# Optimization experiments

Hardware: AMD Instinct MI355X
Metric: run time of the kernel (lower is better)

The kernel has to match this reference:

```python
import jax, jax.numpy as jnp
import numpy as np

B, L, D, H = 2, 2048, 1024, 16
DK = D // H


def setup_inputs() -> dict:
    key = jax.random.key(0)
    ks = jax.random.split(key, 12)
    s = 1.0 / np.sqrt(D)
    return {
        "x": jax.random.normal(ks[0], (B, L, D), jnp.float32),
        "timestamps": jnp.sort(jax.random.uniform(ks[1], (B, L), jnp.float32) * 1000.0, axis=-1),
        "decay_values": jax.random.normal(ks[2], (B, L), jnp.float32),
        "pad_mask": jnp.ones((B, L), dtype=bool),
        "Wq": jax.random.normal(ks[3], (D, D), jnp.float32) * s,
        "bq": jnp.zeros((D,), jnp.float32),
        "Wk": jax.random.normal(ks[4], (D, D), jnp.float32) * s,
        "bk": jnp.zeros((D,), jnp.float32),
        "Wv": jax.random.normal(ks[5], (D, D), jnp.float32) * s,
        "bv": jnp.zeros((D,), jnp.float32),
        "Wo": jax.random.normal(ks[6], (D, D), jnp.float32) * s,
        "bo": jnp.zeros((D,), jnp.float32),
        "lam": jnp.float32(0.01),
    }


def reference(x, timestamps, decay_values, pad_mask, Wq, bq, Wk, bk, Wv, bv, Wo, bo, lam):
    b, l, d = x.shape
    # projections (torch Linear: x @ W.T + b), split heads -> [B,H,L,DK]
    def split_heads(y):
        return y.reshape(b, l, H, DK).transpose(0, 2, 1, 3)
    Q = split_heads(x @ Wq.T + bq)
    K = split_heads(x @ Wk.T + bk)
    V = split_heads(x @ Wv.T + bv)

    scores = jnp.einsum("bhqd,bhkd->bhqk", Q, K) / np.sqrt(DK)
    # temporal log-decay bias
    t_diff = jnp.abs(timestamps[:, :, None] - timestamps[:, None, :])  # [B,L,L]
    denom = jax.lax.stop_gradient(jnp.maximum(t_diff.max(), 1.0))  # matches .item() constant
    scores = scores - jnp.abs(lam) * jnp.log1p(t_diff / denom)[:, None, :, :]

    causal = jnp.triu(jnp.ones((l, l), dtype=bool), k=1)  # True above diag -> masked
    neg_inf = jnp.float32(-jnp.inf)
    scores = jnp.where(causal[None, None], neg_inf, scores)
    scores = jnp.where(pad_mask[:, None, None, :], scores, neg_inf)

    attn = jnp.nan_to_num(jax.nn.softmax(scores, axis=-1), nan=0.0)
    out = jnp.einsum("bhqk,bhkd->bhqd", attn, V)
    out = out.transpose(0, 2, 1, 3).reshape(b, l, d)
    return out @ Wo.T + bo
```

## Files before the change

kernel.cpp:

```cpp
#include <hip/hip_runtime.h>
#include <hip/hip_bf16.h>
#include <math.h>

#define Bsz 2
#define Lsz 2048
#define Dsz 1024
#define Hsz 16
#define DKsz 64
#define NW_ELEMS (1u << 20)

typedef __attribute__((ext_vector_type(8))) short short8;
typedef __attribute__((ext_vector_type(4))) float v4f;
typedef unsigned short ushortT;
#define MFMA16(a, b, c) __builtin_amdgcn_mfma_f32_16x16x32_bf16(a, b, c, 0, 0, 0)
#define LOG2E 1.44269504088896340736f

__device__ __forceinline__ ushortT f2bf(float f) {
    union { float f; unsigned u; } x; x.f = f;
    unsigned r = x.u + 0x7fffu + ((x.u >> 16) & 1u);
    return (ushortT)(r >> 16);
}
__device__ __forceinline__ float bf2f(ushortT s) {
    union { unsigned u; float f; } x; x.u = ((unsigned)s) << 16;
    return x.f;
}
__device__ __forceinline__ void glds16(const void* g, void* l) {
    __builtin_amdgcn_global_load_lds(
        (const __attribute__((address_space(1))) void*)g,
        (__attribute__((address_space(3))) void*)l, 16, 0, 0);
}

__global__ __launch_bounds__(256) void cast_all(const float* __restrict__ x,
                                                const float* __restrict__ Wq,
                                                const float* __restrict__ Wk,
                                                const float* __restrict__ Wv,
                                                const float* __restrict__ Wo,
                                                ushortT* __restrict__ xb,
                                                ushortT* __restrict__ Wqkvb,
                                                ushortT* __restrict__ Wob) {
    const int NX = Bsz * Lsz * Dsz;
    int i = (blockIdx.x * 256 + threadIdx.x) * 4;
    const float* src; ushortT* dst;
    if (i < NX) { src = x + i; dst = xb + i; }
    else {
        int j = i - NX;
        if (j < 3 * (int)NW_ELEMS) {
            int w = j >> 20, o = j & (NW_ELEMS - 1);
            src = (w == 0 ? Wq : (w == 1 ? Wk : Wv)) + o;
            dst = Wqkvb + j;
        } else {
            int o = j - 3 * NW_ELEMS;
            src = Wo + o; dst = Wob + o;
        }
    }
    float4 v = *(const float4*)src;
    ushort4 o4;
    o4.x = f2bf(v.x); o4.y = f2bf(v.y); o4.z = f2bf(v.z); o4.w = f2bf(v.w);
    *(ushort4*)dst = o4;
}

__global__ __launch_bounds__(256) void denom_bias_kernel(const float* __restrict__ t,
                                                         const float* __restrict__ bq,
                                                         const float* __restrict__ bk,
                                                         const float* __restrict__ bv,
                                                         float* __restrict__ out,
                                                         float* __restrict__ cbias) {
    __shared__ float smx[256], smn[256];
    int tid = threadIdx.x;
    for (int i = tid; i < 3 * Dsz; i += 256)
        cbias[i] = (i < Dsz) ? bq[i] : (i < 2 * Dsz ? bk[i - Dsz] : bv[i - 2 * Dsz]);
    float best = 1.0f;
    for (int b = 0; b < Bsz; ++b) {
        float mx = -INFINITY, mn = INFINITY;
        for (int i = tid; i < Lsz; i += 256) {
            float v = t[b * Lsz + i];
            mx = fmaxf(mx, v);
            mn = fminf(mn, v);
        }
        smx[tid] = mx; smn[tid] = mn;
        __syncthreads();
        for (int s = 128; s > 0; s >>= 1) {
            if (tid < s) {
                smx[tid] = fmaxf(smx[tid], smx[tid + s]);
                smn[tid] = fminf(smn[tid], smn[tid + s]);
            }
            __syncthreads();
        }
        best = fmaxf(best, smx[0] - smn[0]);
        __syncthreads();
    }
    if (tid == 0) out[0] = best;
}

template <bool QKV>
__global__ __launch_bounds__(256) void gemm_mfma(const ushortT* __restrict__ A,
                                                 const ushortT* __restrict__ W,
                                                 const float* __restrict__ bias,
                                                 void* __restrict__ O0,
                                                 void* __restrict__ O1,
                                                 void* __restrict__ O2) {
    const int K = Dsz;
    __shared__ ushortT As[128 * 32];
    __shared__ ushortT Ws[128 * 32];
    int tid = threadIdx.x;
    int wid = tid >> 6, lane = tid & 63, quad = lane >> 4, m16 = lane & 15;
    int wm = wid >> 1, wn = wid & 1;
    int m0 = blockIdx.y * 128, n0 = blockIdx.x * 128;
    int lrow = lane >> 2, lcol = (lane & 3) * 8;

    v4f acc[4][4];
#pragma unroll
    for (int i = 0; i < 4; ++i)
#pragma unroll
        for (int j = 0; j < 4; ++j) acc[i][j] = (v4f){0.f, 0.f, 0.f, 0.f};

    for (int kt = 0; kt < K; kt += 32) {
        __syncthreads();
#pragma unroll
        for (int hf = 0; hf < 2; ++hf) {
            int r0 = wid * 32 + hf * 16;
            const ushortT* ga = A + (size_t)(m0 + r0 + lrow) * K + kt + lcol;
            const ushortT* gw = W + (size_t)(n0 + r0 + lrow) * K + kt + lcol;
            glds16(ga, &As[r0 * 32]);
            glds16(gw, &Ws[r0 * 32]);
        }
        __syncthreads();
        short8 af[4], wf[4];
#pragma unroll
        for (int mt = 0; mt < 4; ++mt)
            af[mt] = *(const short8*)&As[(wm * 64 + mt * 16 + m16) * 32 + quad * 8];
#pragma unroll
        for (int nt = 0; nt < 4; ++nt)
            wf[nt] = *(const short8*)&Ws[(wn * 64 + nt * 16 + m16) * 32 + quad * 8];
#pragma unroll
        for (int mt = 0; mt < 4; ++mt)
#pragma unroll
            for (int nt = 0; nt < 4; ++nt)
                acc[mt][nt] = MFMA16(af[mt], wf[nt], acc[mt][nt]);
    }

    if (QKV) {
        int region = n0 >> 10;
        float scale = (region == 0) ? 0.125f * LOG2E : 1.0f;
#pragma unroll
        for (int nt = 0; nt < 4; ++nt) {
            int col = n0 + wn * 64 + nt * 16 + m16;
            float bv_ = bias[col];
            int c1 = col & (Dsz - 1);
#pragma unroll
            for (int mt = 0; mt < 4; ++mt) {
                int row0 = m0 + wm * 64 + mt * 16 + quad * 4;
                if (region == 2) {
                    ushort4 pk;
                    pk.x = f2bf(acc[mt][nt][0] + bv_);
                    pk.y = f2bf(acc[mt][nt][1] + bv_);
                    pk.z = f2bf(acc[mt][nt][2] + bv_);
                    pk.w = f2bf(acc[mt][nt][3] + bv_);
                    int bb = row0 >> 11, seq = row0 & (Lsz - 1);
                    *(ushort4*)&((ushortT*)O2)[((size_t)bb * Dsz + c1) * Lsz + seq] = pk;
                } else {
                    ushortT* dst = (ushortT*)(region == 0 ? O0 : O1);
#pragma unroll
                    for (int r = 0; r < 4; ++r)
                        dst[(size_t)(row0 + r) * Dsz + c1] =
                            f2bf((acc[mt][nt][r] + bv_) * scale);
                }
            }
        }
    } else {
#pragma unroll
        for (int nt = 0; nt < 4; ++nt) {
            int col = n0 + wn * 64 + nt * 16 + m16;
            float bv_ = bias[col];
#pragma unroll
            for (int mt = 0; mt < 4; ++mt) {
                int row0 = m0 + wm * 64 + mt * 16 + quad * 4;
#pragma unroll
                for (int r = 0; r < 4; ++r)
                    ((float*)O0)[(size_t)(row0 + r) * Dsz + col] = acc[mt][nt][r] + bv_;
            }
        }
    }
}

__global__ __launch_bounds__(512) void attn_mfma(const ushortT* __restrict__ Qb,
                                                 const ushortT* __restrict__ Kb,
                                                 const ushortT* __restrict__ Vtg,
                                                 const float* __restrict__ ts,
                                                 const float* __restrict__ denomp,
                                                 const float* __restrict__ lamp,
                                                 ushortT* __restrict__ AOb) {
    int pid = blockIdx.x;
    int h = blockIdx.y, b = blockIdx.z;
    int tid = threadIdx.x;
    int wid = tid >> 6, lane = tid & 63, quad = lane >> 4, m16 = lane & 15;

    __shared__ ushortT Ks[64 * 72];
    __shared__ ushortT Vs[64 * 72];
    __shared__ ushortT Pl[8][16 * 72];
    __shared__ float tks[64];

    float denom = denomp[0];
    float alam = fabsf(lamp[0]);
    float c0 = alam * __builtin_amdgcn_logf(denom);
    const size_t bL = (size_t)b * Lsz;

    int sr = tid >> 3, sc = (tid & 7) * 8;

    for (int half = 0; half < 2; ++half) {
        int qt = half ? (15 - pid) : pid;
        int q0 = qt * 128;
        int ntiles = 2 * (qt + 1);
        int jd = 2 * qt + (wid >> 2);

        int qrow = q0 + wid * 16 + m16;
        const ushortT* qptr = Qb + (bL + qrow) * Dsz + h * 64 + quad * 8;
        short8 qf0 = *(const short8*)qptr;
        short8 qf1 = *(const short8*)(qptr + 32);

        float tq[4];
        int gq[4];
#pragma unroll
        for (int r = 0; r < 4; ++r) {
            gq[r] = q0 + wid * 16 + quad * 4 + r;
            tq[r] = ts[bL + gq[r]];
        }

        v4f o[4];
        float lacc[4];
#pragma unroll
        for (int i = 0; i < 4; ++i) { o[i] = (v4f){0.f, 0.f, 0.f, 0.f}; lacc[i] = 0.f; }

        uint4 kv, vv;
        float tkv = 0.f;
        {
            const ushortT* ksrc = Kb + (bL + sr) * Dsz + h * 64 + sc;
            const ushortT* vsrc = Vtg + ((size_t)b * Dsz + h * 64 + sr) * Lsz + sc;
            kv = *(const uint4*)ksrc;
            vv = *(const uint4*)vsrc;
            if (tid < 64) tkv = ts[bL + tid];
        }

        for (int jt = 0; jt < ntiles; ++jt) {
            int k0 = jt * 64;
            __syncthreads();
            *(uint4*)&Ks[sr * 72 + sc] = kv;
            *(uint4*)&Vs[sr * 72 + sc] = vv;
            if (tid < 64) tks[tid] = tkv;
            __syncthreads();
            if (jt + 1 < ntiles) {
                int k1 = k0 + 64;
                const ushortT* ksrc = Kb + (bL + k1 + sr) * Dsz + h * 64 + sc;
                const ushortT* vsrc = Vtg + ((size_t)b * Dsz + h * 64 + sr) * Lsz + k1 + sc;
                kv = *(const uint4*)ksrc;
                vv = *(const uint4*)vsrc;
                if (tid < 64) tkv = ts[bL + k1 + tid];
            }
            if (jt > jd) continue;

            v4f s[4];
#pragma unroll
            for (int ct = 0; ct < 4; ++ct) {
                short8 kf0 = *(const short8*)&Ks[(ct * 16 + m16) * 72 + quad * 8];
                short8 kf1 = *(const short8*)&Ks[(ct * 16 + m16) * 72 + 32 + quad * 8];
                s[ct] = (v4f){0.f, 0.f, 0.f, 0.f};
                s[ct] = MFMA16(qf0, kf0, s[ct]);
                s[ct] = MFMA16(qf1, kf1, s[ct]);
            }

            bool diag = (jt == jd);
#pragma unroll
            for (int ct = 0; ct < 4; ++ct) {
                int gk = k0 + ct * 16 + m16;
                float tk = tks[ct * 16 + m16];
#pragma unroll
                for (int r = 0; r < 4; ++r) {
                    float w = denom + fabsf(tq[r] - tk);
                    float f = s[ct][r] + fmaf(-alam, __builtin_amdgcn_logf(w), c0);
                    if (diag) f = (gk <= gq[r]) ? f : -INFINITY;
                    float p = __builtin_amdgcn_exp2f(f);
                    ushortT pb = f2bf(p);
                    Pl[wid][(quad * 4 + r) * 72 + ct * 16 + m16] = pb;
                    lacc[r] += bf2f(pb);
                }
            }

            short8 pf0 = *(const short8*)&Pl[wid][m16 * 72 + quad * 8];
            short8 pf1 = *(const short8*)&Pl[wid][m16 * 72 + 32 + quad * 8];
#pragma unroll
            for (int dt = 0; dt < 4; ++dt) {
                short8 vf0 = *(const short8*)&Vs[(dt * 16 + m16) * 72 + quad * 8];
                short8 vf1 = *(const short8*)&Vs[(dt * 16 + m16) * 72 + 32 + quad * 8];
                o[dt] = MFMA16(pf0, vf0, o[dt]);
                o[dt] = MFMA16(pf1, vf1, o[dt]);
            }
        }

#pragma unroll
        for (int r = 0; r < 4; ++r) {
            float l = lacc[r];
#pragma unroll
            for (int off = 1; off < 16; off <<= 1)
                l += __shfl_xor(l, off, 16);
            float invl = 1.0f / l;
#pragma unroll
            for (int dt = 0; dt < 4; ++dt) {
                int col = h * 64 + dt * 16 + m16;
                AOb[(bL + gq[r]) * Dsz + col] = f2bf(o[dt][r] * invl);
            }
        }
    }
}

extern "C" void kernel_launch(void* const* d_in, const int* in_sizes, int n_in,
                              void* d_out, int out_size, void* d_ws, size_t ws_size,
                              hipStream_t stream) {
    const float* x   = (const float*)d_in[0];
    const float* ts  = (const float*)d_in[1];
    const float* Wq  = (const float*)d_in[4];
    const float* bq  = (const float*)d_in[5];
    const float* Wk  = (const float*)d_in[6];
    const float* bk  = (const float*)d_in[7];
    const float* Wv  = (const float*)d_in[8];
    const float* bv  = (const float*)d_in[9];
    const float* Wo  = (const float*)d_in[10];
    const float* bo  = (const float*)d_in[11];
    const float* lam = (const float*)d_in[12];

    const size_t NX = (size_t)Bsz * Lsz * Dsz;
    const size_t NW = (size_t)NW_ELEMS;

    char* w = (char*)d_ws;
    float* denom = (float*)w;            w += 256;
    float* cbias = (float*)w;            w += 3 * Dsz * 4 + 256;
    ushortT* xb    = (ushortT*)w;        w += NX * 2;
    ushortT* Wqkvb = (ushortT*)w;        w += 3 * NW * 2;
    ushortT* Wob   = (ushortT*)w;        w += NW * 2;
    ushortT* Qb    = (ushortT*)w;        w += NX * 2;
    ushortT* Kbf   = (ushortT*)w;        w += NX * 2;
    ushortT* Vtg   = (ushortT*)w;        w += NX * 2;
    ushortT* AOb   = (ushortT*)w;        w += NX * 2;

    denom_bias_kernel<<<1, 256, 0, stream>>>(ts, bq, bk, bv, denom, cbias);

    int cast_blocks = (int)((NX + 4 * NW) / 4 / 256);
    cast_all<<<cast_blocks, 256, 0, stream>>>(x, Wq, Wk, Wv, Wo, xb, Wqkvb, Wob);

    dim3 gqkv(3 * Dsz / 128, (Bsz * Lsz) / 128);
    gemm_mfma<true><<<gqkv, 256, 0, stream>>>(xb, Wqkvb, cbias, Qb, Kbf, Vtg);

    dim3 ablk(8, Hsz, Bsz);
    attn_mfma<<<ablk, 512, 0, stream>>>(Qb, Kbf, Vtg, ts, denom, lam, AOb);

    dim3 gout(Dsz / 128, (Bsz * Lsz) / 128);
    gemm_mfma<false><<<gout, 256, 0, stream>>>(AOb, Wob, bo, d_out, nullptr, nullptr);
}
```

Baseline: 242.9 us.

## Shrink attention blocks to 64-row tiles and fuse denom into cast kernel

The attention kernel moves from 512-thread blocks over 128-query tiles to 256-thread blocks over 64-query tiles, doubling the grid and removing idle warps that skipped the last key tile. The denominator/bias reduction runs as an extra block of the cast kernel, saving one launch. The bf16 conversion of probabilities now truncates instead of rounding to nearest, and the bias add is folded into a single FMA. Truncation changes numerics slightly, and the smaller blocks reload K/V tiles more often per query.

```diff
diff --git a/kernel.cpp b/kernel.cpp
--- a/kernel.cpp
+++ b/kernel.cpp
@@ -20,26 +20,57 @@
     unsigned r = x.u + 0x7fffu + ((x.u >> 16) & 1u);
     return (ushortT)(r >> 16);
 }
-__device__ __forceinline__ float bf2f(ushortT s) {
-    union { unsigned u; float f; } x; x.u = ((unsigned)s) << 16;
-    return x.f;
-}
 __device__ __forceinline__ void glds16(const void* g, void* l) {
     __builtin_amdgcn_global_load_lds(
         (const __attribute__((address_space(1))) void*)g,
         (__attribute__((address_space(3))) void*)l, 16, 0, 0);
 }
 
-__global__ __launch_bounds__(256) void cast_all(const float* __restrict__ x,
-                                                const float* __restrict__ Wq,
-                                                const float* __restrict__ Wk,
-                                                const float* __restrict__ Wv,
-                                                const float* __restrict__ Wo,
-                                                ushortT* __restrict__ xb,
-                                                ushortT* __restrict__ Wqkvb,
-                                                ushortT* __restrict__ Wob) {
+__global__ __launch_bounds__(256) void cast_denom(const float* __restrict__ x,
+                                                  const float* __restrict__ Wq,
+                                                  const float* __restrict__ Wk,
+                                                  const float* __restrict__ Wv,
+                                                  const float* __restrict__ Wo,
+                                                  const float* __restrict__ t,
+                                                  const float* __restrict__ bq,
+                                                  const float* __restrict__ bk,
+                                                  const float* __restrict__ bv,
+                                                  ushortT* __restrict__ xb,
+                                                  ushortT* __restrict__ Wqkvb,
+                                                  ushortT* __restrict__ Wob,
+                                                  float* __restrict__ denom_out,
+                                                  float* __restrict__ cbias,
+                                                  int ncast) {
     const int NX = Bsz * Lsz * Dsz;
-    int i = (blockIdx.x * 256 + threadIdx.x) * 4;
+    int tid = threadIdx.x;
+    if ((int)blockIdx.x == ncast) {
+        __shared__ float smx[256], smn[256];
+        for (int i = tid; i < 3 * Dsz; i += 256)
+            cbias[i] = (i < Dsz) ? bq[i] : (i < 2 * Dsz ? bk[i - Dsz] : bv[i - 2 * Dsz]);
+        float best = 1.0f;
+        for (int b = 0; b < Bsz; ++b) {
+            float mx = -INFINITY, mn = INFINITY;
+            for (int i = tid; i < Lsz; i += 256) {
+                float v = t[b * Lsz + i];
+                mx = fmaxf(mx, v);
+                mn = fminf(mn, v);
+            }
+            smx[tid] = mx; smn[tid] = mn;
+            __syncthreads();
+            for (int s = 128; s > 0; s >>= 1) {
+                if (tid < s) {
+                    smx[tid] = fmaxf(smx[tid], smx[tid + s]);
+                    smn[tid] = fminf(smn[tid], smn[tid + s]);
+                }
+                __syncthreads();
+            }
+            best = fmaxf(best, smx[0] - smn[0]);
+            __syncthreads();
+        }
+        if (tid == 0) denom_out[0] = best;
+        return;
+    }
+    int i = (blockIdx.x * 256 + tid) * 4;
     const float* src; ushortT* dst;
     if (i < NX) { src = x + i; dst = xb + i; }
     else {
@@ -57,39 +88,6 @@
     ushort4 o4;
     o4.x = f2bf(v.x); o4.y = f2bf(v.y); o4.z = f2bf(v.z); o4.w = f2bf(v.w);
     *(ushort4*)dst = o4;
-}
-
-__global__ __launch_bounds__(256) void denom_bias_kernel(const float* __restrict__ t,
-                                                         const float* __restrict__ bq,
-                                                         const float* __restrict__ bk,
-                                                         const float* __restrict__ bv,
-                                                         float* __restrict__ out,
-                                                         float* __restrict__ cbias) {
-    __shared__ float smx[256], smn[256];
-    int tid = threadIdx.x;
-    for (int i = tid; i < 3 * Dsz; i += 256)
-        cbias[i] = (i < Dsz) ? bq[i] : (i < 2 * Dsz ? bk[i - Dsz] : bv[i - 2 * Dsz]);
-    float best = 1.0f;
-    for (int b = 0; b < Bsz; ++b) {
-        float mx = -INFINITY, mn = INFINITY;
-        for (int i = tid; i < Lsz; i += 256) {
-            float v = t[b * Lsz + i];
-            mx = fmaxf(mx, v);
-            mn = fminf(mn, v);
-        }
-        smx[tid] = mx; smn[tid] = mn;
-        __syncthreads();
-        for (int s = 128; s > 0; s >>= 1) {
-            if (tid < s) {
-                smx[tid] = fmaxf(smx[tid], smx[tid + s]);
-                smn[tid] = fminf(smn[tid], smn[tid + s]);
-            }
-            __syncthreads();
-        }
-        best = fmaxf(best, smx[0] - smn[0]);
-        __syncthreads();
-    }
-    if (tid == 0) out[0] = best;
 }
 
 template <bool QKV>
@@ -183,7 +181,7 @@
     }
 }
 
-__global__ __launch_bounds__(512) void attn_mfma(const ushortT* __restrict__ Qb,
+__global__ __launch_bounds__(256) void attn_mfma(const ushortT* __restrict__ Qb,
                                                  const ushortT* __restrict__ Kb,
                                                  const ushortT* __restrict__ Vtg,
                                                  const float* __restrict__ ts,
@@ -197,7 +195,7 @@
 
     __shared__ ushortT Ks[64 * 72];
     __shared__ ushortT Vs[64 * 72];
-    __shared__ ushortT Pl[8][16 * 72];
+    __shared__ ushortT Pl[4][16 * 72];
     __shared__ float tks[64];
 
     float denom = denomp[0];
@@ -205,13 +203,12 @@
     float c0 = alam * __builtin_amdgcn_logf(denom);
     const size_t bL = (size_t)b * Lsz;
 
-    int sr = tid >> 3, sc = (tid & 7) * 8;
+    int sr = tid >> 2, sc = (tid & 3) * 16;
 
     for (int half = 0; half < 2; ++half) {
-        int qt = half ? (15 - pid) : pid;
-        int q0 = qt * 128;
-        int ntiles = 2 * (qt + 1);
-        int jd = 2 * qt + (wid >> 2);
+        int qt = half ? (31 - pid) : pid;
+        int q0 = qt * 64;
+        int ntiles = qt + 1;
 
         int qrow = q0 + wid * 16 + m16;
         const ushortT* qptr = Qb + (bL + qrow) * Dsz + h * 64 + quad * 8;
@@ -231,32 +228,31 @@
 #pragma unroll
         for (int i = 0; i < 4; ++i) { o[i] = (v4f){0.f, 0.f, 0.f, 0.f}; lacc[i] = 0.f; }
 
-        uint4 kv, vv;
+        uint4 kv0, kv1, vv0, vv1;
         float tkv = 0.f;
         {
             const ushortT* ksrc = Kb + (bL + sr) * Dsz + h * 64 + sc;
             const ushortT* vsrc = Vtg + ((size_t)b * Dsz + h * 64 + sr) * Lsz + sc;
-            kv = *(const uint4*)ksrc;
-            vv = *(const uint4*)vsrc;
+            kv0 = *(const uint4*)ksrc; kv1 = *(const uint4*)(ksrc + 8);
+            vv0 = *(const uint4*)vsrc; vv1 = *(const uint4*)(vsrc + 8);
             if (tid < 64) tkv = ts[bL + tid];
         }
 
         for (int jt = 0; jt < ntiles; ++jt) {
             int k0 = jt * 64;
             __syncthreads();
-            *(uint4*)&Ks[sr * 72 + sc] = kv;
-            *(uint4*)&Vs[sr * 72 + sc] = vv;
+            *(uint4*)&Ks[sr * 72 + sc] = kv0; *(uint4*)&Ks[sr * 72 + sc + 8] = kv1;
+            *(uint4*)&Vs[sr * 72 + sc] = vv0; *(uint4*)&Vs[sr * 72 + sc + 8] = vv1;
             if (tid < 64) tks[tid] = tkv;
             __syncthreads();
             if (jt + 1 < ntiles) {
                 int k1 = k0 + 64;
                 const ushortT* ksrc = Kb + (bL + k1 + sr) * Dsz + h * 64 + sc;
                 const ushortT* vsrc = Vtg + ((size_t)b * Dsz + h * 64 + sr) * Lsz + k1 + sc;
-                kv = *(const uint4*)ksrc;
-                vv = *(const uint4*)vsrc;
+                kv0 = *(const uint4*)ksrc; kv1 = *(const uint4*)(ksrc + 8);
+                vv0 = *(const uint4*)vsrc; vv1 = *(const uint4*)(vsrc + 8);
                 if (tid < 64) tkv = ts[bL + k1 + tid];
             }
-            if (jt > jd) continue;
 
             v4f s[4];
 #pragma unroll
@@ -268,7 +264,7 @@
                 s[ct] = MFMA16(qf1, kf1, s[ct]);
             }
 
-            bool diag = (jt == jd);
+            bool diag = (jt == qt);
 #pragma unroll
             for (int ct = 0; ct < 4; ++ct) {
                 int gk = k0 + ct * 16 + m16;
@@ -276,12 +272,12 @@
 #pragma unroll
                 for (int r = 0; r < 4; ++r) {
                     float w = denom + fabsf(tq[r] - tk);
-                    float f = s[ct][r] + fmaf(-alam, __builtin_amdgcn_logf(w), c0);
+                    float f = fmaf(-alam, __builtin_amdgcn_logf(w), s[ct][r] + c0);
                     if (diag) f = (gk <= gq[r]) ? f : -INFINITY;
                     float p = __builtin_amdgcn_exp2f(f);
-                    ushortT pb = f2bf(p);
-                    Pl[wid][(quad * 4 + r) * 72 + ct * 16 + m16] = pb;
-                    lacc[r] += bf2f(pb);
+                    unsigned pu = __builtin_bit_cast(unsigned, p);
+                    Pl[wid][(quad * 4 + r) * 72 + ct * 16 + m16] = (ushortT)(pu >> 16);
+                    lacc[r] += __builtin_bit_cast(float, pu & 0xffff0000u);
                 }
             }
 
@@ -341,16 +337,15 @@
     ushortT* Vtg   = (ushortT*)w;        w += NX * 2;
     ushortT* AOb   = (ushortT*)w;        w += NX * 2;
 
-    denom_bias_kernel<<<1, 256, 0, stream>>>(ts, bq, bk, bv, denom, cbias);
-
-    int cast_blocks = (int)((NX + 4 * NW) / 4 / 256);
-    cast_all<<<cast_blocks, 256, 0, stream>>>(x, Wq, Wk, Wv, Wo, xb, Wqkvb, Wob);
+    int ncast = (int)((NX + 4 * NW) / 4 / 256);
+    cast_denom<<<ncast + 1, 256, 0, stream>>>(x, Wq, Wk, Wv, Wo, ts, bq, bk, bv,
+                                              xb, Wqkvb, Wob, denom, cbias, ncast);
 
     dim3 gqkv(3 * Dsz / 128, (Bsz * Lsz) / 128);
     gemm_mfma<true><<<gqkv, 256, 0, stream>>>(xb, Wqkvb, cbias, Qb, Kbf, Vtg);
 
-    dim3 ablk(8, Hsz, Bsz);
-    attn_mfma<<<ablk, 512, 0, stream>>>(Qb, Kbf, Vtg, ts, denom, lam, AOb);
+    dim3 ablk(16, Hsz, Bsz);
+    attn_mfma<<<ablk, 256, 0, stream>>>(Qb, Kbf, Vtg, ts, denom, lam, AOb);
 
     dim3 gout(Dsz / 128, (Bsz * Lsz) / 128);
     gemm_mfma<false><<<gout, 256, 0, stream>>>(AOb, Wob, bo, d_out, nullptr, nullptr);
```

Measured after the change: 242.1 us. No clear change (-0.3%).
